# Kernel optimization log

Hardware: AMD Instinct MI355X
Metric: run time of the kernel (lower is better)

The kernel has to match this reference:

```python
import jax, jax.numpy as jnp
import numpy as np

# IO parameters (aihwkit-style preset)
INP_BOUND = 1.0
INP_RES = 1.0 / 254.0      # 8-bit DAC: 2^8 - 2 levels
OUT_BOUND = 12.0
OUT_RES = 1.0 / 510.0      # 9-bit ADC: 2^9 - 2 levels
OUT_NOISE = 0.06
OUT_SCALE = 1.0
MAX_BM_FACTOR = 1000.0
MAX_BM_RES = 0.25
INP_RES_EFF = 2.0 * INP_BOUND * INP_RES  # effective input grid step (bm escape test)


def _quantize_st(x, res, bound):
    # UniformQuantize: round to grid of step (res * 2 * bound), straight-through grad
    r = (1.0 / res if res > 1.0 else res) * 2.0 * bound
    q = jnp.round(x / r) * r
    return x + jax.lax.stop_gradient(q - x)


def _one_pass(input_, weight, nm, reduction, rnd, key):
    """One analog MVM pass at a given bound-management reduction factor."""
    scale = 1.0 / (nm * reduction)                      # [m, 1]
    x = input_ * scale                                  # noise/bound managed input
    x = _quantize_st(x, INP_RES, INP_BOUND)             # DAC discretization
    x = jnp.clip(x, -INP_BOUND, INP_BOUND)              # DAC clipping
    out = x @ weight.T                                  # [m, out_size] analog GEMM
    noise = OUT_NOISE * jax.random.normal(
        jax.random.fold_in(key, rnd), out.shape, out.dtype)
    out = out + noise                                   # output (ADC) noise
    out = _quantize_st(out, OUT_RES, OUT_BOUND)         # ADC discretization
    not_clipping = jnp.all((out <= OUT_BOUND) & (out >= -OUT_BOUND))
    out = jnp.clip(out, -OUT_BOUND, OUT_BOUND)          # ADC saturation
    return not_clipping, out


def setup_inputs() -> dict:
    key = jax.random.key(0)
    k1, k2 = jax.random.split(key)
    input_ = jax.random.normal(k1, (8192, 4096), jnp.float32)
    # 0.1 std weights -> outputs mostly within ADC bound after 1-2 bm rounds
    weight = 0.1 * jax.random.normal(k2, (4096, 4096), jnp.float32)
    return {"input_": input_, "weight": weight}


def reference(input_, weight):
    key = jax.random.key(42)
    # noise management: ABS_MAX over the input dimension (nm_thres <= 0 -> no clamp)
    nm = jnp.max(jnp.abs(input_), axis=-1, keepdims=True)
    nm = jnp.where(nm <= 0.0, 1.0, nm)
    out_shape = input_.shape[:-1] + (weight.shape[0],)

    def cond(c):
        return ~c[2]

    def body(c):
        rnd, red, _, _ = c
        red = red * 2.0          # reduction_due_to_bound_management *= 2
        rnd = rnd + 1
        passed, out = _one_pass(input_, weight, nm, red, rnd, key)
        passed = passed | (red > MAX_BM_FACTOR) | (red > MAX_BM_RES / INP_RES_EFF)
        return (rnd, red, passed, out)

    init = (jnp.int32(0), jnp.float32(0.5), jnp.array(False),
            jnp.zeros(out_shape, input_.dtype))
    _, red, _, out = jax.lax.while_loop(cond, body, init)
    # undo the input scaling: output *= out_scale / scale = out_scale * nm * red
    return out * (OUT_SCALE * nm * red)
```

## Files before the change

kernel.cpp:

```cpp
#include <hip/hip_runtime.h>
#include <stdint.h>


#define MM 8192
#define KK 4096
#define NN 4096
#define TOTAL_OUT ((size_t)MM * (size_t)NN)
#define NT (KK / 64)

typedef __attribute__((ext_vector_type(4))) float f32x4;
typedef __attribute__((ext_vector_type(8))) short bf16x8;
typedef __attribute__((ext_vector_type(8))) unsigned short u16x8;

#define R_IN_F ((float)(2.0 / 254.0))
#define R_OUT_F ((float)(24.0 / 510.0))

struct BmState {
  int viol[8];
};

__host__ __device__ __forceinline__ uint32_t tf_rotl(uint32_t v, int r) {
  return (v << r) | (v >> (32 - r));
}

__host__ __device__ __forceinline__ void threefry2x32(uint32_t k0, uint32_t k1,
                                                      uint32_t x0, uint32_t x1,
                                                      uint32_t &o0, uint32_t &o1) {
  uint32_t ks2 = k0 ^ k1 ^ 0x1BD11BDAu;
  x0 += k0; x1 += k1;
#define TF_R(r) { x0 += x1; x1 = tf_rotl(x1, r); x1 ^= x0; }
  TF_R(13) TF_R(15) TF_R(26) TF_R(6)
  x0 += k1; x1 += ks2 + 1u;
  TF_R(17) TF_R(29) TF_R(16) TF_R(24)
  x0 += ks2; x1 += k0 + 2u;
  TF_R(13) TF_R(15) TF_R(26) TF_R(6)
  x0 += k0; x1 += k1 + 3u;
  TF_R(17) TF_R(29) TF_R(16) TF_R(24)
  x0 += k1; x1 += ks2 + 4u;
  TF_R(13) TF_R(15) TF_R(26) TF_R(6)
  x0 += ks2; x1 += k0 + 5u;
#undef TF_R
  o0 = x0; o1 = x1;
}

__device__ __forceinline__ float erfinv_xla(float x) {
  float w = -log1pf(-x * x);
  float p;
  if (w < 5.0f) {
    w = w - 2.5f;
    p = 2.81022636e-08f;
    p = fmaf(p, w, 3.43273939e-07f);
    p = fmaf(p, w, -3.5233877e-06f);
    p = fmaf(p, w, -4.39150654e-06f);
    p = fmaf(p, w, 0.00021858087f);
    p = fmaf(p, w, -0.00125372503f);
    p = fmaf(p, w, -0.00417768164f);
    p = fmaf(p, w, 0.246640727f);
    p = fmaf(p, w, 1.50140941f);
  } else {
    w = sqrtf(w) - 3.0f;
    p = -0.000200214257f;
    p = fmaf(p, w, 0.000100950558f);
    p = fmaf(p, w, 0.00134934322f);
    p = fmaf(p, w, -0.00367342844f);
    p = fmaf(p, w, 0.00573950773f);
    p = fmaf(p, w, -0.0076224613f);
    p = fmaf(p, w, 0.00943887047f);
    p = fmaf(p, w, 1.00167406f);
    p = fmaf(p, w, 2.83297682f);
  }
  return p * x;
}

__device__ __forceinline__ float noise_from_bits(uint32_t bits) {
  uint32_t fb = (bits >> 9) | 0x3f800000u;
  float f = __uint_as_float(fb) - 1.0f;
  const float lo = -0.99999994f;
  float u = f * 2.0f + lo;
  u = fmaxf(lo, u);
  return 0.06f * (1.41421356f * erfinv_xla(u));
}

__device__ __forceinline__ unsigned short bf16_rne(float f) {
  uint32_t x = __float_as_uint(f);
  x += 0x7fffu + ((x >> 16) & 1u);
  return (unsigned short)(x >> 16);
}

__device__ __forceinline__ float dac_quant(float v, float s) {
  float x = v * s;
  float t = x / R_IN_F;
  float k = rintf(t);
  return fminf(127.0f, fmaxf(-127.0f, k));
}

__device__ __forceinline__ u16x8 quant8(float4 a, float4 b, float s) {
  u16x8 o;
  o[0] = bf16_rne(dac_quant(a.x, s));
  o[1] = bf16_rne(dac_quant(a.y, s));
  o[2] = bf16_rne(dac_quant(a.z, s));
  o[3] = bf16_rne(dac_quant(a.w, s));
  o[4] = bf16_rne(dac_quant(b.x, s));
  o[5] = bf16_rne(dac_quant(b.y, s));
  o[6] = bf16_rne(dac_quant(b.z, s));
  o[7] = bf16_rne(dac_quant(b.w, s));
  return o;
}

__device__ __forceinline__ u16x8 conv8(float4 a, float4 b) {
  u16x8 o;
  o[0] = bf16_rne(a.x); o[1] = bf16_rne(a.y); o[2] = bf16_rne(a.z); o[3] = bf16_rne(a.w);
  o[4] = bf16_rne(b.x); o[5] = bf16_rne(b.y); o[6] = bf16_rne(b.z); o[7] = bf16_rne(b.w);
  return o;
}

__device__ __forceinline__ float adc_one(float gval, size_t idx, float sc,
                                         uint32_t fk0, uint32_t fk1, bool &bad) {
  uint32_t w0, w1;
  threefry2x32(fk0, fk1, 0u, (uint32_t)idx, w0, w1);
  float o = R_IN_F * gval + noise_from_bits(w0 ^ w1);
  float q = rintf(o / R_OUT_F) * R_OUT_F;
  float z = o + (q - o);
  bad = bad || (z > 12.0f) || (z < -12.0f);
  z = fminf(12.0f, fmaxf(-12.0f, z));
  return z * sc;
}

__device__ __forceinline__ bool pass_skipped(const BmState *st, int pass) {
  for (int q = 1; q < pass; ++q)
    if (st->viol[q] == 0) return true;
  return false;
}

__global__ __launch_bounds__(256) void k_prep(const float *__restrict__ in,
                                              const float *__restrict__ w,
                                              float *__restrict__ nm,
                                              unsigned short *__restrict__ ab,
                                              unsigned short *__restrict__ wb,
                                              BmState *st) {
  const int t = threadIdx.x;
  if (blockIdx.x < MM) {
    if (blockIdx.x == 0 && t == 0) {
      for (int i = 0; i < 8; ++i) st->viol[i] = 0;
    }
    const int row = blockIdx.x;
    const float *r = in + (size_t)row * KK;
    float4 a0 = *(const float4 *)(r + t * 8);
    float4 a1 = *(const float4 *)(r + t * 8 + 4);
    float4 b0 = *(const float4 *)(r + 2048 + t * 8);
    float4 b1 = *(const float4 *)(r + 2048 + t * 8 + 4);
    float m = 0.0f;
    m = fmaxf(m, fmaxf(fmaxf(fabsf(a0.x), fabsf(a0.y)), fmaxf(fabsf(a0.z), fabsf(a0.w))));
    m = fmaxf(m, fmaxf(fmaxf(fabsf(a1.x), fabsf(a1.y)), fmaxf(fabsf(a1.z), fabsf(a1.w))));
    m = fmaxf(m, fmaxf(fmaxf(fabsf(b0.x), fabsf(b0.y)), fmaxf(fabsf(b0.z), fabsf(b0.w))));
    m = fmaxf(m, fmaxf(fmaxf(fabsf(b1.x), fabsf(b1.y)), fmaxf(fabsf(b1.z), fabsf(b1.w))));
#pragma unroll
    for (int off = 32; off > 0; off >>= 1) m = fmaxf(m, __shfl_down(m, off));
    __shared__ float wm[4];
    if ((t & 63) == 0) wm[t >> 6] = m;
    __syncthreads();
    const float mm = fmaxf(fmaxf(wm[0], wm[1]), fmaxf(wm[2], wm[3]));
    const float nmv = (mm <= 0.0f) ? 1.0f : mm;
    if (t == 0) nm[row] = nmv;
    const float s = 1.0f / (nmv * 1.0f);
    unsigned short *o = ab + (size_t)row * KK;
    *(u16x8 *)(o + t * 8) = quant8(a0, a1, s);
    *(u16x8 *)(o + 2048 + t * 8) = quant8(b0, b1, s);
  } else {
    const size_t idx = ((size_t)(blockIdx.x - MM) * 256 + t) * 8;
    float4 a = *(const float4 *)(w + idx);
    float4 b = *(const float4 *)(w + idx + 4);
    *(u16x8 *)(wb + idx) = conv8(a, b);
  }
}

__global__ __launch_bounds__(256) void k_rowmax(const float *__restrict__ in,
                                                float *__restrict__ nm, BmState *st) {
  if (blockIdx.x == 0 && threadIdx.x == 0) {
    for (int i = 0; i < 8; ++i) st->viol[i] = 0;
  }
  const int row = blockIdx.x;
  const float4 *r = (const float4 *)(in + (size_t)row * KK);
  const int t = threadIdx.x;
  float m = 0.0f;
#pragma unroll
  for (int i = 0; i < 4; ++i) {
    float4 v = r[t + i * 256];
    m = fmaxf(m, fmaxf(fmaxf(fabsf(v.x), fabsf(v.y)), fmaxf(fabsf(v.z), fabsf(v.w))));
  }
#pragma unroll
  for (int off = 32; off > 0; off >>= 1) m = fmaxf(m, __shfl_down(m, off));
  __shared__ float wm[4];
  if ((t & 63) == 0) wm[t >> 6] = m;
  __syncthreads();
  if (t == 0) {
    m = fmaxf(fmaxf(wm[0], wm[1]), fmaxf(wm[2], wm[3]));
    nm[row] = (m <= 0.0f) ? 1.0f : m;
  }
}

__device__ __forceinline__ void async16(const void *g, void *l) {
  __builtin_amdgcn_global_load_lds((const __attribute__((address_space(1))) uint32_t *)g,
                                   (__attribute__((address_space(3))) uint32_t *)l,
                                   16, 0, 0);
}

__global__ __launch_bounds__(512, 1) void k_gemm(const unsigned short *__restrict__ A,
                                                 const unsigned short *__restrict__ B,
                                                 float *__restrict__ C) {
  __shared__ unsigned short As[2][256 * 64];
  __shared__ unsigned short Bs[2][256 * 64];
  const int tid = threadIdx.x;
  const int lane = tid & 63;
  const int wv = tid >> 6;
  const int wr = wv >> 2;
  const int wc = wv & 3;
  const int brow = blockIdx.y * 256;
  const int bcol = blockIdx.x * 256;

  f32x4 acc[8][4];
#pragma unroll
  for (int m = 0; m < 8; ++m)
#pragma unroll
    for (int n = 0; n < 4; ++n) acc[m][n] = (f32x4){0.f, 0.f, 0.f, 0.f};

  int sr[4], sk8[4];
#pragma unroll
  for (int i = 0; i < 4; ++i) {
    const int u = i * 512 + tid;
    sr[i] = u >> 3;
    sk8[i] = ((u & 7) ^ (sr[i] & 7)) * 8;
  }

#define STAGE(buf, kt)                                                                 \
  {                                                                                    \
    _Pragma("unroll") for (int i = 0; i < 4; ++i) {                                    \
      const int ub = i * 512 + wv * 64;                \
      async16(A + (size_t)(brow + sr[i]) * KK + (kt) * 64 + sk8[i],                    \
              (char *)As[buf] + (size_t)ub * 16);                                      \
      async16(B + (size_t)(bcol + sr[i]) * KK + (kt) * 64 + sk8[i],                    \
              (char *)Bs[buf] + (size_t)ub * 16);                                      \
    }                                                                                  \
  }

  STAGE(0, 0);

  const int r16 = lane & 15;
  const int kg = (lane >> 4) * 8;

#pragma unroll 2
  for (int kt = 0; kt < NT; ++kt) {
    const int cur = kt & 1;
    if (kt + 1 < NT) {
      STAGE(cur ^ 1, kt + 1);
      asm volatile("s_waitcnt vmcnt(8)" ::: "memory");
    } else {
      asm volatile("s_waitcnt vmcnt(0)" ::: "memory");
    }
    __builtin_amdgcn_s_barrier();

#pragma unroll
    for (int kk = 0; kk < 64; kk += 32) {
      const int ck = (kk + kg) >> 3;
      bf16x8 af[8], bg[4];
#pragma unroll
      for (int m = 0; m < 8; ++m) {
        const int ra = wr * 128 + m * 16 + r16;
        af[m] = *(const bf16x8 *)(As[cur] + ra * 64 + ((ck ^ (ra & 7)) << 3));
      }
#pragma unroll
      for (int n = 0; n < 4; ++n) {
        const int rb = wc * 64 + n * 16 + r16;
        bg[n] = *(const bf16x8 *)(Bs[cur] + rb * 64 + ((ck ^ (rb & 7)) << 3));
      }
#pragma unroll
      for (int m = 0; m < 8; ++m)
#pragma unroll
        for (int n = 0; n < 4; ++n)
          acc[m][n] = __builtin_amdgcn_mfma_f32_16x16x32_bf16(af[m], bg[n], acc[m][n], 0, 0, 0);
    }
    __builtin_amdgcn_sched_barrier(0);
    __builtin_amdgcn_s_barrier();
  }
#undef STAGE

  const int c16 = lane & 15;
  const int q4 = (lane >> 4) * 4;
#pragma unroll
  for (int m = 0; m < 8; ++m) {
    const int row = brow + wr * 128 + m * 16 + q4;
#pragma unroll
    for (int n = 0; n < 4; ++n) {
      const int col = bcol + wc * 64 + n * 16 + c16;
      float *cp = C + (size_t)row * NN + col;
      cp[0 * (size_t)NN] = acc[m][n][0];
      cp[1 * (size_t)NN] = acc[m][n][1];
      cp[2 * (size_t)NN] = acc[m][n][2];
      cp[3 * (size_t)NN] = acc[m][n][3];
    }
  }
}

__global__ __launch_bounds__(256) void k_epi(float *__restrict__ out,
                                             const float *__restrict__ nm,
                                             BmState *__restrict__ st, int pass, float red,
                                             uint32_t fk0, uint32_t fk1) {
  const size_t idx = ((size_t)blockIdx.x * 256 + threadIdx.x) * 8;
  const int row = (int)(idx >> 12);
  const float sc = nm[row] * red;
  float4 a = *(const float4 *)(out + idx);
  float4 b = *(const float4 *)(out + idx + 4);
  float v[8] = {a.x, a.y, a.z, a.w, b.x, b.y, b.z, b.w};
  bool bad = false;
#pragma unroll
  for (int j = 0; j < 8; ++j) v[j] = adc_one(v[j], idx + j, sc, fk0, fk1, bad);
  *(float4 *)(out + idx) = make_float4(v[0], v[1], v[2], v[3]);
  *(float4 *)(out + idx + 4) = make_float4(v[4], v[5], v[6], v[7]);
  unsigned long long vb = __ballot(bad ? 1 : 0);
  if (vb != 0ull && (threadIdx.x & 63) == 0) atomicOr(&st->viol[pass], 1);
}

__global__ __launch_bounds__(256) void k_retry(const float *__restrict__ Af,
                                               const float *__restrict__ Bf,
                                               const float *__restrict__ nm, float red,
                                               float *__restrict__ C,
                                               BmState *__restrict__ st, int pass,
                                               uint32_t fk0, uint32_t fk1) {
  if (pass_skipped(st, pass)) return;
  __shared__ unsigned short As[128 * 64];
  __shared__ unsigned short Bs[128 * 64];
  const int tid = threadIdx.x;
  const int lane = tid & 63;
  const int wv = tid >> 6;
  const int wr = wv >> 1, wc = wv & 1;
  const int brow = blockIdx.y * 128;
  const int bcol = blockIdx.x * 128;

  f32x4 acc[4][4];
#pragma unroll
  for (int m = 0; m < 4; ++m)
#pragma unroll
    for (int n = 0; n < 4; ++n) acc[m][n] = (f32x4){0.f, 0.f, 0.f, 0.f};

  float sA[4];
#pragma unroll
  for (int i = 0; i < 4; ++i) {
    int u = i * 256 + tid;
    sA[i] = 1.0f / (nm[brow + (u >> 3)] * red);
  }

  for (int kt = 0; kt < KK; kt += 64) {
#pragma unroll
    for (int i = 0; i < 4; ++i) {
      const int u = i * 256 + tid;
      const int r = u >> 3, k8 = (u & 7) * 8;
      {
        const float *g = Af + (size_t)(brow + r) * KK + kt + k8;
        float4 x = *(const float4 *)g, y = *(const float4 *)(g + 4);
        *(u16x8 *)(As + r * 64 + k8) = quant8(x, y, sA[i]);
      }
      {
        const float *g = Bf + (size_t)(bcol + r) * KK + kt + k8;
        float4 x = *(const float4 *)g, y = *(const float4 *)(g + 4);
        *(u16x8 *)(Bs + r * 64 + k8) = conv8(x, y);
      }
    }
    __syncthreads();

    const int r16 = lane & 15;
    const int kg = (lane >> 4) * 8;
#pragma unroll
    for (int kk = 0; kk < 64; kk += 32) {
      bf16x8 af[4], bg[4];
#pragma unroll
      for (int m = 0; m < 4; ++m)
        af[m] = *(const bf16x8 *)(As + (wr * 64 + m * 16 + r16) * 64 + kk + kg);
#pragma unroll
      for (int n = 0; n < 4; ++n)
        bg[n] = *(const bf16x8 *)(Bs + (wc * 64 + n * 16 + r16) * 64 + kk + kg);
#pragma unroll
      for (int m = 0; m < 4; ++m)
#pragma unroll
        for (int n = 0; n < 4; ++n)
          acc[m][n] = __builtin_amdgcn_mfma_f32_16x16x32_bf16(af[m], bg[n], acc[m][n], 0, 0, 0);
    }
    __syncthreads();
  }

  const int c16 = lane & 15;
  const int q4 = (lane >> 4) * 4;
  bool bad = false;
#pragma unroll
  for (int m = 0; m < 4; ++m) {
    const int row0 = brow + wr * 64 + m * 16 + q4;
#pragma unroll
    for (int j = 0; j < 4; ++j) {
      const int row = row0 + j;
      const float sc = nm[row] * red;
#pragma unroll
      for (int n = 0; n < 4; ++n) {
        const int col = bcol + wc * 64 + n * 16 + c16;
        const size_t idx = (size_t)row * NN + col;
        C[idx] = adc_one(acc[m][n][j], idx, sc, fk0, fk1, bad);
      }
    }
  }
  unsigned long long vb = __ballot(bad ? 1 : 0);
  if (vb != 0ull && (threadIdx.x & 63) == 0) atomicOr(&st->viol[pass], 1);
}

extern "C" void kernel_launch(void *const *d_in, const int *in_sizes, int n_in,
                              void *d_out, int out_size, void *d_ws, size_t ws_size,
                              hipStream_t stream) {
  const float *input = (const float *)d_in[0];
  const float *weight = (const float *)d_in[1];
  if (n_in >= 2 && in_sizes[0] < in_sizes[1]) {
    const float *t = input; input = weight; weight = t;
  }
  float *out = (float *)d_out;
  char *ws = (char *)d_ws;
  BmState *st = (BmState *)ws;
  float *nm = (float *)(ws + 4096);
  unsigned short *Ab = (unsigned short *)(ws + 36864);
  unsigned short *Wb = Ab + (size_t)MM * KK;
  const size_t need = 36864 + ((size_t)MM * KK + (size_t)NN * KK) * 2;
  const bool fast = ws_size >= need;

  uint32_t fk[8][2];
  for (int p = 1; p <= 6; ++p) threefry2x32(0u, 42u, 0u, (uint32_t)p, fk[p][0], fk[p][1]);

  if (fast) {
    k_prep<<<dim3(MM + (NN * (size_t)KK) / 2048), dim3(256), 0, stream>>>(
        input, weight, nm, Ab, Wb, st);
    k_gemm<<<dim3(NN / 256, MM / 256), dim3(512), 0, stream>>>(Ab, Wb, out);
    k_epi<<<dim3((int)(TOTAL_OUT / 2048)), dim3(256), 0, stream>>>(out, nm, st, 1, 1.0f,
                                                                   fk[1][0], fk[1][1]);
  } else {
    k_rowmax<<<dim3(MM), dim3(256), 0, stream>>>(input, nm, st);
    k_retry<<<dim3(NN / 128, MM / 128), dim3(256), 0, stream>>>(
        input, weight, nm, 1.0f, out, st, 1, fk[1][0], fk[1][1]);
  }

  float red = 2.0f;
  for (int p = 2; p <= 6; ++p, red *= 2.0f) {
    k_retry<<<dim3(NN / 128, MM / 128), dim3(256), 0, stream>>>(
        input, weight, nm, red, out, st, p, fk[p][0], fk[p][1]);
  }
}
```

Before: 489.3 us.

## Interleave GEMM global loads with MFMA phases using split half-tile staging

```diff
diff --git a/kernel.cpp b/kernel.cpp
--- a/kernel.cpp
+++ b/kernel.cpp
@@ -208,8 +208,8 @@
 __global__ __launch_bounds__(512, 1) void k_gemm(const unsigned short *__restrict__ A,
                                                  const unsigned short *__restrict__ B,
                                                  float *__restrict__ C) {
-  __shared__ unsigned short As[2][256 * 64];
-  __shared__ unsigned short Bs[2][256 * 64];
+  __shared__ unsigned short As[2][2][128 * 64];
+  __shared__ unsigned short Bs[2][2][128 * 64];
   const int tid = threadIdx.x;
   const int lane = tid & 63;
   const int wv = tid >> 6;
@@ -224,65 +224,93 @@
 #pragma unroll
     for (int n = 0; n < 4; ++n) acc[m][n] = (f32x4){0.f, 0.f, 0.f, 0.f};
 
-  int sr[4], sk8[4];
-#pragma unroll
-  for (int i = 0; i < 4; ++i) {
+  int srow[2], scg[2], sub[2];
+#pragma unroll
+  for (int i = 0; i < 2; ++i) {
     const int u = i * 512 + tid;
-    sr[i] = u >> 3;
-    sk8[i] = ((u & 7) ^ (sr[i] & 7)) * 8;
-  }
-
-#define STAGE(buf, kt)                                                                 \
+    srow[i] = u >> 3;
+    scg[i] = ((u & 7) ^ (srow[i] & 7)) * 8;
+    sub[i] = i * 512 + wv * 64;
+  }
+  const unsigned short *gA[2] = {A + (size_t)brow * KK, A + (size_t)(brow + 128) * KK};
+  const unsigned short *gB[2] = {B + (size_t)bcol * KK, B + (size_t)(bcol + 128) * KK};
+
+#define SHALF(dst, src, ktile)                                                         \
   {                                                                                    \
-    _Pragma("unroll") for (int i = 0; i < 4; ++i) {                                    \
-      const int ub = i * 512 + wv * 64;                \
-      async16(A + (size_t)(brow + sr[i]) * KK + (kt) * 64 + sk8[i],                    \
-              (char *)As[buf] + (size_t)ub * 16);                                      \
-      async16(B + (size_t)(bcol + sr[i]) * KK + (kt) * 64 + sk8[i],                    \
-              (char *)Bs[buf] + (size_t)ub * 16);                                      \
+    _Pragma("unroll") for (int i_ = 0; i_ < 2; ++i_) {                                 \
+      async16((src) + (size_t)srow[i_] * KK + (size_t)(ktile) * 64 + scg[i_],          \
+              (char *)(dst) + (size_t)sub[i_] * 16);                                   \
     }                                                                                  \
   }
 
-  STAGE(0, 0);
+  SHALF(As[0][0], gA[0], 0)
+  SHALF(As[0][1], gA[1], 0)
+  SHALF(Bs[0][0], gB[0], 0)
+  SHALF(Bs[0][1], gB[1], 0)
+  asm volatile("s_waitcnt vmcnt(0)" ::: "memory");
+  __builtin_amdgcn_s_barrier();
 
   const int r16 = lane & 15;
-  const int kg = (lane >> 4) * 8;
+  const int kgc = lane >> 4;
+  const int hB = wc >> 1;
+  const int rB0 = (wc & 1) * 64;
 
 #pragma unroll 2
   for (int kt = 0; kt < NT; ++kt) {
-    const int cur = kt & 1;
-    if (kt + 1 < NT) {
-      STAGE(cur ^ 1, kt + 1);
-      asm volatile("s_waitcnt vmcnt(8)" ::: "memory");
-    } else {
-      asm volatile("s_waitcnt vmcnt(0)" ::: "memory");
-    }
-    __builtin_amdgcn_s_barrier();
-
-#pragma unroll
-    for (int kk = 0; kk < 64; kk += 32) {
-      const int ck = (kk + kg) >> 3;
-      bf16x8 af[8], bg[4];
-#pragma unroll
-      for (int m = 0; m < 8; ++m) {
-        const int ra = wr * 128 + m * 16 + r16;
-        af[m] = *(const bf16x8 *)(As[cur] + ra * 64 + ((ck ^ (ra & 7)) << 3));
-      }
-#pragma unroll
-      for (int n = 0; n < 4; ++n) {
-        const int rb = wc * 64 + n * 16 + r16;
-        bg[n] = *(const bf16x8 *)(Bs[cur] + rb * 64 + ((ck ^ (rb & 7)) << 3));
-      }
-#pragma unroll
-      for (int m = 0; m < 8; ++m)
-#pragma unroll
-        for (int n = 0; n < 4; ++n)
-          acc[m][n] = __builtin_amdgcn_mfma_f32_16x16x32_bf16(af[m], bg[n], acc[m][n], 0, 0, 0);
-    }
-    __builtin_amdgcn_sched_barrier(0);
-    __builtin_amdgcn_s_barrier();
-  }
-#undef STAGE
+    const int p = kt & 1;
+    bf16x8 bg[2][4];
+#pragma unroll
+    for (int q = 0; q < 4; ++q) {
+      bf16x8 af[2][2];
+#pragma unroll
+      for (int x = 0; x < 2; ++x)
+#pragma unroll
+        for (int mm = 0; mm < 2; ++mm) {
+          const int ra = (2 * q + mm) * 16 + r16;
+          af[x][mm] = *(const bf16x8 *)(&As[p][wr][ra * 64 +
+                                                   (((x * 4 + kgc) ^ (ra & 7)) << 3)]);
+        }
+      if (q == 0) {
+#pragma unroll
+        for (int x = 0; x < 2; ++x)
+#pragma unroll
+          for (int n = 0; n < 4; ++n) {
+            const int rb = rB0 + n * 16 + r16;
+            bg[x][n] = *(const bf16x8 *)(&Bs[p][hB][rb * 64 +
+                                                    (((x * 4 + kgc) ^ (rb & 7)) << 3)]);
+          }
+      }
+      if (kt + 1 < NT) {
+        const int pn = p ^ 1;
+        if (q == 0) { SHALF(As[pn][0], gA[0], kt + 1) }
+        else if (q == 1) { SHALF(As[pn][1], gA[1], kt + 1) }
+        else if (q == 2) { SHALF(Bs[pn][0], gB[0], kt + 1) }
+        else { SHALF(Bs[pn][1], gB[1], kt + 1) }
+      }
+      if (q == 0) asm volatile("s_waitcnt lgkmcnt(8)" ::: "memory");
+      __builtin_amdgcn_s_barrier();
+      asm volatile("s_waitcnt lgkmcnt(0)" ::: "memory");
+      __builtin_amdgcn_sched_barrier(0);
+      __builtin_amdgcn_s_setprio(1);
+#pragma unroll
+      for (int x = 0; x < 2; ++x)
+#pragma unroll
+        for (int mm = 0; mm < 2; ++mm)
+#pragma unroll
+          for (int n = 0; n < 4; ++n)
+            acc[2 * q + mm][n] = __builtin_amdgcn_mfma_f32_16x16x32_bf16(
+                af[x][mm], bg[x][n], acc[2 * q + mm][n], 0, 0, 0);
+      __builtin_amdgcn_s_setprio(0);
+      if (q < 3) {
+        __builtin_amdgcn_s_barrier();
+      } else {
+        __builtin_amdgcn_sched_barrier(0);
+        asm volatile("s_waitcnt vmcnt(0)" ::: "memory");
+        __builtin_amdgcn_s_barrier();
+      }
+    }
+  }
+#undef SHALF
 
   const int c16 = lane & 15;
   const int q4 = (lane >> 4) * 4;
```

Result: no change. 493.7 us (+0.9%).
